# Kernel optimization log

Measured on AMD Instinct MI355X. Metric: run time of the kernel, lower is better.

The kernel has to match this reference:

```python
import jax, jax.numpy as jnp
import numpy as np

N = 30000; E = 480000; B = 32
IN_H = 129; IN_P = 15; HID = 64; HEADS = 8; OUT = 129


def gat_conv(x, src, dst, edge_attr, W, a_src, a_dst, We, a_e, bias, concat):
    # PyG GATConv with edge_dim, add_self_loops=True (fill_value='mean'), negative_slope=0.2
    n = x.shape[0]
    H, C = a_src.shape
    ones = jnp.ones((src.shape[0],), x.dtype)
    deg = jax.ops.segment_sum(ones, dst, num_segments=n)
    ea_mean = jax.ops.segment_sum(edge_attr, dst, num_segments=n) / jnp.clip(deg, 1.0)[:, None]
    loop = jnp.arange(n, dtype=src.dtype)
    s = jnp.concatenate([src, loop])
    t = jnp.concatenate([dst, loop])
    ea = jnp.concatenate([edge_attr, ea_mean], axis=0)
    xw = (x @ W).reshape(n, H, C)              # [N,H,C]
    a_s = jnp.sum(xw * a_src, axis=-1)         # [N,H]
    a_d = jnp.sum(xw * a_dst, axis=-1)         # [N,H]
    ew = (ea @ We).reshape(-1, H, C)           # [E2,H,C]
    a_ed = jnp.sum(ew * a_e, axis=-1)          # [E2,H]
    alpha = jax.nn.leaky_relu(a_s[s] + a_d[t] + a_ed, 0.2)
    amax = jax.ops.segment_max(alpha, t, num_segments=n)   # every node has a self-loop
    expa = jnp.exp(alpha - amax[t])
    denom = jax.ops.segment_sum(expa, t, num_segments=n)
    alpha = expa / denom[t]                    # segment softmax over dst
    out = jax.ops.segment_sum(xw[s] * alpha[..., None], t, num_segments=n)  # [N,H,C]
    out = out.reshape(n, H * C) if concat else jnp.mean(out, axis=1)
    return out + bias


def setup_inputs():
    key = jax.random.key(0)
    ks = jax.random.split(key, 40)
    g = lambda k, s: (jax.random.normal(k, s, jnp.float32) * (1.0 / np.sqrt(s[0])))
    d = {}
    d['x_hrtf'] = jax.random.normal(ks[0], (N, IN_H), jnp.float32)
    d['x_pos'] = jax.random.normal(ks[1], (N, IN_P), jnp.float32)
    d['edge_attr_hrtf'] = jax.random.normal(ks[2], (E, 1), jnp.float32)
    d['edge_attr_pos'] = jax.random.normal(ks[3], (E, 1), jnp.float32)
    # hrtf branch, layer 1 (heads=8, concat)
    d['W1h'] = g(ks[4], (IN_H, HEADS * HID)); d['as1h'] = g(ks[5], (HEADS, HID)); d['ad1h'] = g(ks[6], (HEADS, HID))
    d['We1h'] = g(ks[7], (1, HEADS * HID)); d['ae1h'] = g(ks[8], (HEADS, HID)); d['b1h'] = jnp.zeros((HEADS * HID,), jnp.float32)
    # hrtf branch, layer 2 (heads=1, mean)
    d['W2h'] = g(ks[9], (HEADS * HID, OUT)); d['as2h'] = g(ks[10], (1, OUT)); d['ad2h'] = g(ks[11], (1, OUT))
    d['We2h'] = g(ks[12], (1, OUT)); d['ae2h'] = g(ks[13], (1, OUT)); d['b2h'] = jnp.zeros((OUT,), jnp.float32)
    # pos branch, layer 1
    d['W1p'] = g(ks[14], (IN_P, HEADS * HID)); d['as1p'] = g(ks[15], (HEADS, HID)); d['ad1p'] = g(ks[16], (HEADS, HID))
    d['We1p'] = g(ks[17], (1, HEADS * HID)); d['ae1p'] = g(ks[18], (HEADS, HID)); d['b1p'] = jnp.zeros((HEADS * HID,), jnp.float32)
    # pos branch, layer 2
    d['W2p'] = g(ks[19], (HEADS * HID, OUT)); d['as2p'] = g(ks[20], (1, OUT)); d['ad2p'] = g(ks[21], (1, OUT))
    d['We2p'] = g(ks[22], (1, OUT)); d['ae2p'] = g(ks[23], (1, OUT)); d['b2p'] = jnp.zeros((OUT,), jnp.float32)
    # final fc
    d['Wfc'] = g(ks[24], (2 * OUT, 129)); d['bfc'] = jnp.zeros((129,), jnp.float32)
    d['edge_index_hrtf'] = jax.random.randint(ks[25], (2, E), 0, N, jnp.int32)
    d['edge_index_pos'] = jax.random.randint(ks[26], (2, E), 0, N, jnp.int32)
    d['batch'] = ((jnp.arange(N) * B) // N).astype(jnp.int32)  # sorted, equal-sized graphs
    d['num_graphs'] = B
    return d


def reference(x_hrtf, x_pos, edge_attr_hrtf, edge_attr_pos, W1h, as1h, ad1h, We1h, ae1h, b1h, W2h, as2h, ad2h, We2h, ae2h, b2h, W1p, as1p, ad1p, We1p, ae1p, b1p, W2p, as2p, ad2p, We2p, ae2p, b2p, Wfc, bfc, edge_index_hrtf, edge_index_pos, batch, num_graphs):
    sh, th = edge_index_hrtf[0], edge_index_hrtf[1]
    sp, tp = edge_index_pos[0], edge_index_pos[1]
    h = jax.nn.elu(gat_conv(x_hrtf, sh, th, edge_attr_hrtf, W1h, as1h, ad1h, We1h, ae1h, b1h, True))
    h = gat_conv(h, sh, th, edge_attr_hrtf, W2h, as2h, ad2h, We2h, ae2h, b2h, False)
    p = jax.nn.elu(gat_conv(x_pos, sp, tp, edge_attr_pos, W1p, as1p, ad1p, We1p, ae1p, b1p, True))
    p = gat_conv(p, sp, tp, edge_attr_pos, W2p, as2p, ad2p, We2p, ae2p, b2p, False)
    counts = jax.ops.segment_sum(jnp.ones_like(batch), batch, num_segments=num_graphs)
    last = jnp.cumsum(counts) - 1              # last node index of each graph
    z = jnp.concatenate([h[last], p[last]], axis=-1)
    z = z @ Wfc + bfc
    return z[:, None, :]                       # [B,1,129]
```

## Files before the change

### kernel.cpp

```cpp
#include <hip/hip_runtime.h>

#define N_NODES 30000
#define N_EDGES 480000
#define NB      32
#define HEADS   8
#define F1      512
#define OUT_C   129
#define OUT_S   132
#define W1TS    132

#define CAP1   1024
#define MAXD   64
#define NZREG  (8 + 2 * CAP1 + 2 * NB)
#define TJ     32
#define RB     8

#define SHIFT1 12.0f
#define SHIFT2 20.0f

__device__ __forceinline__ float lrelu(float a) { return a > 0.f ? a : 0.2f * a; }

__device__ __forceinline__ int graph_of(int v) { return (int)(((unsigned)v * 2u) / 1875u); }
__device__ __forceinline__ int last_of(int b) { return (int)((((unsigned)(b + 1) * 1875u) + 1u) / 2u) - 1; }
__device__ __forceinline__ bool is_last_node(int v) { return v == last_of(graph_of(v)); }

__global__ void k_prep(const float* We1h, const float* ae1h,
                       const float* We1p, const float* ae1p,
                       const float* We2h, const float* ae2h,
                       const float* We2p, const float* ae2p,
                       const float* __restrict__ W1h, const float* __restrict__ W1p,
                       const float* __restrict__ W2h, const float* __restrict__ W2p,
                       const float* as1h, const float* as1p,
                       const float* ad1h, const float* ad1p,
                       float* k12, float* __restrict__ w_as, float* __restrict__ w_ad,
                       float* __restrict__ W2t2, int* __restrict__ zreg,
                       int* __restrict__ inv1) {
    int gid = blockIdx.x * 256 + threadIdx.x;
    if (gid < 15000) ((int4*)inv1)[gid] = make_int4(-1, -1, -1, -1);
    if (gid < NZREG) zreg[gid] = 0;
    if (gid < 512 * OUT_C) {
        int k = gid / OUT_C, c = gid % OUT_C;
        W2t2[c * 512 + k] = W2h[gid];
        W2t2[512 * OUT_C + c * 512 + k] = W2p[gid];
    }
    if (blockIdx.x == 0) {
        int t = threadIdx.x;
        if (t < 8) {
            float s = 0.f;
            for (int c = 0; c < 64; c++) s += We1h[t * 64 + c] * ae1h[t * 64 + c];
            k12[t] = s;
        } else if (t < 16) {
            int h = t - 8;
            float s = 0.f;
            for (int c = 0; c < 64; c++) s += We1p[h * 64 + c] * ae1p[h * 64 + c];
            k12[8 + h] = s;
        } else if (t == 16) {
            float s = 0.f;
            for (int c = 0; c < OUT_C; c++) s += We2h[c] * ae2h[c];
            k12[16] = s;
        } else if (t == 17) {
            float s = 0.f;
            for (int c = 0; c < OUT_C; c++) s += We2p[c] * ae2p[c];
            k12[17] = s;
        }
    }
    if (blockIdx.x >= 128 && blockIdx.x < 160) {
        int bb = blockIdx.x - 128;
        int br = bb >> 4, type = (bb >> 3) & 1, h = bb & 7;
        const float* W1 = br ? W1p : W1h;
        const float* a  = type ? (br ? ad1p : ad1h) : (br ? as1p : as1h);
        float* outp = (type ? w_ad : w_as) + (size_t)(br * 8 + h) * W1TS;
        int K = br ? 15 : 129;
        int d = threadIdx.x;
        if (d < K) {
            float s = 0.f;
            for (int c = 0; c < 64; c++) s += W1[(size_t)d * F1 + h * 64 + c] * a[h * 64 + c];
            outp[d] = s;
        }
    }
}

__global__ __launch_bounds__(256) void k_scan2(const int* __restrict__ ei_h,
        const int* __restrict__ ei_p, const float* __restrict__ ea_h,
        const float* __restrict__ ea_p, int* inv1, int* nodes1, int* cnt,
        int* degcnt2, int* eb2v, float* eb2e) {
    __shared__ int s_claim[128];
    __shared__ int s_n, s_base;
    int br = blockIdx.y;
    const int* ei = br ? ei_p : ei_h;
    const float* ea = br ? ea_p : ea_h;
    const int* src = ei; const int* dst = ei + N_EDGES;
    int* inv1b = inv1 + br * N_NODES;
    int* nodes1b = nodes1 + br * CAP1;
    int* cntp = cnt + br * 4;
    int* dc2 = degcnt2 + br * NB;
    int* e2v = eb2v + br * NB * MAXD;
    float* e2e = eb2e + br * NB * MAXD;
    int tid = threadIdx.x;
    if (tid == 0) s_n = 0;
    __syncthreads();
    auto claim = [&](int v) {
        if (atomicCAS(&inv1b[v], -1, -3) == -1) {
            int p = atomicAdd(&s_n, 1);
            if (p < 128) s_claim[p] = v;
            else {
                int j = atomicAdd(cntp, 1);
                if (j < CAP1) { nodes1b[j] = v; inv1b[v] = j; }
                else inv1b[v] = -1;
            }
        }
    };
    if (blockIdx.x == 0 && tid < NB) claim(last_of(tid));
    int base = (blockIdx.x * 256 + tid) * 4;
    if (base < N_EDGES) {
        int4 d4 = *(const int4*)(dst + base);
        int dv[4] = {d4.x, d4.y, d4.z, d4.w};
#pragma unroll
        for (int q = 0; q < 4; q++) {
            if (is_last_node(dv[q])) {
                int e = base + q;
                int b = graph_of(dv[q]);
                int slot = atomicAdd(dc2 + b, 1);
                if (slot < MAXD) { e2v[b * MAXD + slot] = src[e]; e2e[b * MAXD + slot] = ea[e]; }
                claim(src[e]);
            }
        }
    }
    __syncthreads();
    int n = s_n; if (n > 128) n = 128;
    if (tid == 0) s_base = atomicAdd(cntp, n);
    __syncthreads();
    for (int q = tid; q < n; q += 256) {
        int j = s_base + q;
        int v = s_claim[q];
        if (j < CAP1) { nodes1b[j] = v; inv1b[v] = j; }
        else inv1b[v] = -1;
    }
}

__global__ __launch_bounds__(256) void k_scan1(const int* __restrict__ ei_h,
        const int* __restrict__ ei_p, const float* __restrict__ ea_h,
        const float* __restrict__ ea_p, const int* __restrict__ inv1,
        int* degcnt1, int* ebv1, float* ebe1) {
    int br = blockIdx.y;
    const int* ei = br ? ei_p : ei_h;
    const float* ea = br ? ea_p : ea_h;
    const int* src = ei; const int* dst = ei + N_EDGES;
    const int* inv1b = inv1 + br * N_NODES;
    degcnt1 += br * CAP1; ebv1 += (size_t)br * CAP1 * MAXD; ebe1 += (size_t)br * CAP1 * MAXD;
    int tid = threadIdx.x;
    int base = (blockIdx.x * 256 + tid) * 4;
    if (base >= N_EDGES) return;
    int4 d = *(const int4*)(dst + base);
    int dv[4] = {d.x, d.y, d.z, d.w};
#pragma unroll
    for (int q = 0; q < 4; q++) {
        int jj = inv1b[dv[q]];
        if (jj >= 0 && jj < CAP1) {
            int e = base + q;
            int slot = atomicAdd(degcnt1 + jj, 1);
            if (slot < MAXD) { ebv1[jj * MAXD + slot] = src[e]; ebe1[jj * MAXD + slot] = ea[e]; }
        }
    }
}

__global__ __launch_bounds__(256) void k_agg1(const int* __restrict__ ebv1,
        const float* __restrict__ ebe1, const int* __restrict__ degcnt1,
        const int* __restrict__ nodes1, const int* cnt,
        const float* __restrict__ x_h, const float* __restrict__ x_p,
        const float* __restrict__ w_as, const float* __restrict__ w_ad,
        const float* __restrict__ k12, float* __restrict__ xaggn) {
    __shared__ float s_x[MAXD + 1][W1TS];
    __shared__ int   s_v[MAXD + 1];
    __shared__ float s_e[MAXD + 1];
    __shared__ float s_ex[(MAXD + 1) * 8];
    __shared__ float s_den[8];
    __shared__ float s_adh[8];
    __shared__ float s_k1[8];
    int br = blockIdx.y;
    const float* x    = br ? x_p : x_h;
    const float* wasb = w_as + (size_t)br * 8 * W1TS;
    const float* wadb = w_ad + (size_t)br * 8 * W1TS;
    int K = br ? 15 : 129;
    int n1 = cnt[br * 4 + 0]; if (n1 > CAP1) n1 = CAP1;
    int j = blockIdx.x;
    if (j >= n1) return;
    int tid = threadIdx.x;
    int deg = degcnt1[br * CAP1 + j]; if (deg > MAXD) deg = MAXD;
    const int*   ebv = ebv1 + ((size_t)br * CAP1 + j) * MAXD;
    const float* ebe = ebe1 + ((size_t)br * CAP1 + j) * MAXD;
    if (tid < deg) { s_v[tid] = ebv[tid]; s_e[tid] = ebe[tid]; }
    if (tid == 0) s_v[deg] = nodes1[br * CAP1 + j];
    if (tid >= 72 && tid < 80) s_k1[tid - 72] = k12[br * 8 + (tid - 72)];
    __syncthreads();
    int total = deg + 1;
    for (int k = tid >> 6; k < total; k += 4) {
        const float* xr = x + (size_t)s_v[k] * K;
        for (int d = (tid & 63); d < K; d += 64) s_x[k][d] = xr[d];
    }
    __syncthreads();
    if (tid < 64) {
        float part = (tid < deg) ? s_e[tid] : 0.f;
#pragma unroll
        for (int o = 32; o > 0; o >>= 1) part += __shfl_down(part, o);
        if (tid == 0) s_e[deg] = part / fmaxf((float)deg, 1.f);
    }
    for (int t = tid; t < total * 8 + 8; t += 256) {
        int k, h; const float* wv;
        if (t < total * 8) { k = t >> 3; h = t & 7; wv = wasb + (size_t)h * W1TS; }
        else               { k = total - 1; h = t - total * 8; wv = wadb + (size_t)h * W1TS; }
        float dot = 0.f;
        for (int d = 0; d < K; d++) dot += s_x[k][d] * wv[d];
        if (t < total * 8) s_ex[t] = dot; else s_adh[h] = dot;
    }
    __syncthreads();
    for (int t = tid; t < total * 8; t += 256) {
        int k = t >> 3, h = t & 7;
        float a = lrelu(s_ex[t] + s_adh[h] + s_e[k] * s_k1[h]);
        s_ex[t] = __expf(a - SHIFT1);
    }
    __syncthreads();
    if (tid < 8) {
        float d = 0.f;
        for (int k = 0; k < total; k++) d += s_ex[k * 8 + tid];
        s_den[tid] = 1.f / d;
    }
    __syncthreads();
    if (tid < K) {
        float acc[8];
#pragma unroll
        for (int h = 0; h < 8; h++) acc[h] = 0.f;
        for (int k = 0; k < total; k++) {
            float xv = s_x[k][tid];
#pragma unroll
            for (int h = 0; h < 8; h++) acc[h] += s_ex[k * 8 + h] * xv;
        }
#pragma unroll
        for (int h = 0; h < 8; h++)
            xaggn[((size_t)(br * 8 + h) * CAP1 + j) * W1TS + tid] = acc[h] * s_den[h];
    }
}

__global__ __launch_bounds__(256) void k_h1gemm(const float* __restrict__ xaggn,
        const int* cnt, const float* __restrict__ W1h, const float* __restrict__ W1p,
        const float* __restrict__ b1h, const float* __restrict__ b1p,
        float* __restrict__ h1) {
    __shared__ float s_a[TJ][W1TS];
    __shared__ float s_b[OUT_C][64];
    int br = blockIdx.y;
    const float* W1 = br ? W1p : W1h;
    const float* b1 = br ? b1p : b1h;
    int K = br ? 15 : 129;
    int n1 = cnt[br * 4 + 0]; if (n1 > CAP1) n1 = CAP1;
    int jt = blockIdx.x >> 3, h = blockIdx.x & 7;
    int j0 = jt * TJ;
    if (j0 >= n1) return;
    int tid = threadIdx.x;
    const float4* ap = (const float4*)(xaggn + ((size_t)(br * 8 + h) * CAP1 + j0) * W1TS);
    for (int t = tid; t < TJ * W1TS / 4; t += 256) ((float4*)&s_a[0][0])[t] = ap[t];
    for (int t = tid; t < K * 64; t += 256) {
        int d = t >> 6, c = t & 63;
        s_b[d][c] = W1[(size_t)d * F1 + h * 64 + c];
    }
    __syncthreads();
    int r0 = (tid >> 6) * 8, c = tid & 63;
    float acc[8];
#pragma unroll
    for (int rr = 0; rr < 8; rr++) acc[rr] = 0.f;
    for (int d = 0; d < K; d++) {
        float bv = s_b[d][c];
#pragma unroll
        for (int rr = 0; rr < 8; rr++) acc[rr] += s_a[r0 + rr][d] * bv;
    }
    float bb = b1[h * 64 + c];
#pragma unroll
    for (int rr = 0; rr < 8; rr++) {
        int j = j0 + r0 + rr;
        if (j < n1) {
            float v = acc[rr] + bb;
            h1[((size_t)br * CAP1 + j) * F1 + h * 64 + c] = v > 0.f ? v : (__expf(v) - 1.f);
        }
    }
}

__global__ __launch_bounds__(256) void k_gemm2b(const float* __restrict__ h1,
        const float* __restrict__ W2t2, const float* __restrict__ as2h,
        const float* __restrict__ as2p, const float* __restrict__ ad2h,
        const float* __restrict__ ad2p, const int* cnt,
        float* __restrict__ xw2, float* __restrict__ as2v, float* __restrict__ ad2all) {
    __shared__ float hs[RB][512];
    __shared__ float part[4][RB][132];
    __shared__ float rows_[RB][132];
    __shared__ float redS[4][RB], redD[4][RB];
    int br = blockIdx.y;
    const float* W2t = W2t2 + (size_t)br * 512 * OUT_C;
    const float* as2w = br ? as2p : as2h;
    const float* ad2w = br ? ad2p : ad2h;
    h1 += (size_t)br * CAP1 * F1;
    xw2 += (size_t)br * CAP1 * OUT_S;
    as2v += br * CAP1; ad2all += br * CAP1;
    int n1 = cnt[br * 4 + 0]; if (n1 > CAP1) n1 = CAP1;
    int j0 = blockIdx.x * RB;
    if (j0 >= n1) return;
    int tid = threadIdx.x;
    for (int r = 0; r < RB; r++) {
        int j = j0 + r;
        for (int k = tid; k < 512; k += 256)
            hs[r][k] = (j < n1) ? h1[(size_t)j * F1 + k] : 0.f;
    }
    __syncthreads();
    int w = tid >> 6, l = tid & 63;
    float a0[RB], a1[RB], a2[RB];
#pragma unroll
    for (int r = 0; r < RB; r++) { a0[r] = 0.f; a1[r] = 0.f; a2[r] = 0.f; }
    const float* w0p = W2t + (size_t)l * 512;
    const float* w1p = W2t + (size_t)(64 + l) * 512;
    const float* w2p = W2t + (size_t)128 * 512;
    int kbase = w * 128;
#pragma unroll 2
    for (int kk = 0; kk < 128; kk += 4) {
        int k = kbase + kk;
        float4 wv0 = *(const float4*)(w0p + k);
        float4 wv1 = *(const float4*)(w1p + k);
        float4 wv2 = *(const float4*)(w2p + k);
#pragma unroll
        for (int r = 0; r < RB; r++) {
            float4 hv = *(const float4*)&hs[r][k];
            a0[r] += hv.x * wv0.x + hv.y * wv0.y + hv.z * wv0.z + hv.w * wv0.w;
            a1[r] += hv.x * wv1.x + hv.y * wv1.y + hv.z * wv1.z + hv.w * wv1.w;
            a2[r] += hv.x * wv2.x + hv.y * wv2.y + hv.z * wv2.z + hv.w * wv2.w;
        }
    }
#pragma unroll
    for (int r = 0; r < RB; r++) {
        part[w][r][l] = a0[r];
        part[w][r][64 + l] = a1[r];
        if (l == 0) part[w][r][128] = a2[r];
    }
    __syncthreads();
    for (int idx = tid; idx < RB * OUT_C; idx += 256) {
        int r = idx / OUT_C;
        int c = idx - r * OUT_C;
        float s = part[0][r][c] + part[1][r][c] + part[2][r][c] + part[3][r][c];
        rows_[r][c] = s;
        int j = j0 + r;
        if (j < n1) xw2[(size_t)j * OUT_S + c] = s;
    }
    __syncthreads();
#pragma unroll
    for (int t = 0; t < 2; t++) {
        int r = w + t * 4;
        float ps = rows_[r][l] * as2w[l] + rows_[r][64 + l] * as2w[64 + l];
        float pd = rows_[r][l] * ad2w[l] + rows_[r][64 + l] * ad2w[64 + l];
        if (l == 0) { ps += rows_[r][128] * as2w[128]; pd += rows_[r][128] * ad2w[128]; }
#pragma unroll
        for (int o = 32; o > 0; o >>= 1) { ps += __shfl_down(ps, o); pd += __shfl_down(pd, o); }
        if (l == 0) { redS[w][r] = ps; redD[w][r] = pd; }
    }
    __syncthreads();
    if (tid < RB) {
        int j = j0 + tid;
        if (j < n1) {
            int w0 = tid & 3;
            as2v[j] = redS[w0][tid];
            ad2all[j] = redD[w0][tid];
        }
    }
}

__global__ __launch_bounds__(256) void k_agg2fc(const int* __restrict__ eb2v,
        const float* __restrict__ eb2e, const int* __restrict__ degcnt2,
        const int* __restrict__ inv1, const int* cnt,
        const float* __restrict__ as2v, const float* __restrict__ ad2all,
        const float* __restrict__ k12, const float* __restrict__ b2h,
        const float* __restrict__ b2p, const float* __restrict__ xw2,
        const float* __restrict__ Wfc, const float* __restrict__ bfc,
        float* __restrict__ out) {
    __shared__ int   s_j[MAXD + 1];
    __shared__ float s_e[MAXD + 1];
    __shared__ float s_ex[MAXD + 1];
    __shared__ float s_den;
    __shared__ float hcat[2 * OUT_C];
    int b = blockIdx.x;
    int tid = threadIdx.x;
    for (int br = 0; br < 2; br++) {
        const float* b2 = br ? b2p : b2h;
        const int* inv1b = inv1 + br * N_NODES;
        const float* as2vb = as2v + br * CAP1;
        const float* ad2b = ad2all + br * CAP1;
        const float* xw2b = xw2 + (size_t)br * CAP1 * OUT_S;
        float k2 = k12[16 + br];
        int deg = degcnt2[br * NB + b]; if (deg > MAXD) deg = MAXD;
        if (tid < deg) {
            s_j[tid] = inv1b[eb2v[(br * NB + b) * MAXD + tid]];
            s_e[tid] = eb2e[(br * NB + b) * MAXD + tid];
        }
        if (tid == 0) s_j[deg] = inv1b[last_of(b)];
        __syncthreads();
        if (tid < 64) {
            float part = (tid < deg) ? s_e[tid] : 0.f;
#pragma unroll
            for (int o = 32; o > 0; o >>= 1) part += __shfl_down(part, o);
            if (tid == 0) s_e[deg] = part / fmaxf((float)deg, 1.f);
        }
        __syncthreads();
        int total = deg + 1;
        float adv = ad2b[s_j[deg]];
        for (int k = tid; k < total; k += 256)
            s_ex[k] = __expf(lrelu(as2vb[s_j[k]] + adv + s_e[k] * k2) - SHIFT2);
        __syncthreads();
        if (tid == 0) {
            float d = 0.f;
            for (int k = 0; k < total; k++) d += s_ex[k];
            s_den = d;
        }
        __syncthreads();
        if (tid < OUT_C) {
            float acc = 0.f;
            for (int k = 0; k < total; k++)
                acc += s_ex[k] * xw2b[(size_t)s_j[k] * OUT_S + tid];
            hcat[br * OUT_C + tid] = acc / s_den + b2[tid];
        }
        __syncthreads();
    }
    if (tid < OUT_C) {
        float s = bfc[tid];
        for (int k = 0; k < 2 * OUT_C; k++) s += hcat[k] * Wfc[k * OUT_C + tid];
        out[b * OUT_C + tid] = s;
    }
}

extern "C" void kernel_launch(void* const* d_in, const int* in_sizes, int n_in,
                              void* d_out, int out_size, void* d_ws, size_t ws_size,
                              hipStream_t stream) {
    const float* x_h  = (const float*)d_in[0];
    const float* x_p  = (const float*)d_in[1];
    const float* ea_h = (const float*)d_in[2];
    const float* ea_p = (const float*)d_in[3];
    const float* W1h  = (const float*)d_in[4];
    const float* as1h = (const float*)d_in[5];
    const float* ad1h = (const float*)d_in[6];
    const float* We1h = (const float*)d_in[7];
    const float* ae1h = (const float*)d_in[8];
    const float* b1h  = (const float*)d_in[9];
    const float* W2h  = (const float*)d_in[10];
    const float* as2h = (const float*)d_in[11];
    const float* ad2h = (const float*)d_in[12];
    const float* We2h = (const float*)d_in[13];
    const float* ae2h = (const float*)d_in[14];
    const float* b2h  = (const float*)d_in[15];
    const float* W1p  = (const float*)d_in[16];
    const float* as1p = (const float*)d_in[17];
    const float* ad1p = (const float*)d_in[18];
    const float* We1p = (const float*)d_in[19];
    const float* ae1p = (const float*)d_in[20];
    const float* b1p  = (const float*)d_in[21];
    const float* W2p  = (const float*)d_in[22];
    const float* as2p = (const float*)d_in[23];
    const float* ad2p = (const float*)d_in[24];
    const float* We2p = (const float*)d_in[25];
    const float* ae2p = (const float*)d_in[26];
    const float* b2p  = (const float*)d_in[27];
    const float* Wfc  = (const float*)d_in[28];
    const float* bfc  = (const float*)d_in[29];
    const int*   ei_h = (const int*)d_in[30];
    const int*   ei_p = (const int*)d_in[31];

    char* wsb = (char*)d_ws;
    size_t off = 0;
    auto alloc = [&](size_t elems) -> char* {
        char* p = wsb + off;
        off += ((elems * 4 + 255) / 256) * 256;
        return p;
    };
    float*    k12     = (float*)alloc(18);
    int*      zreg    = (int*)alloc(NZREG);
    int*      cnt     = zreg;
    int*      degcnt1 = zreg + 8;
    int*      degcnt2 = zreg + 8 + 2 * CAP1;
    int*      inv1    = (int*)alloc(2 * N_NODES);
    int*      nodes1  = (int*)alloc(2 * CAP1);
    int*      ebv1    = (int*)alloc(2 * (size_t)CAP1 * MAXD);
    float*    ebe1    = (float*)alloc(2 * (size_t)CAP1 * MAXD);
    int*      eb2v    = (int*)alloc(2 * NB * MAXD);
    float*    eb2e    = (float*)alloc(2 * NB * MAXD);
    float*    w_as    = (float*)alloc(2 * 8 * W1TS);
    float*    w_ad    = (float*)alloc(2 * 8 * W1TS);
    float*    xaggn   = (float*)alloc(2 * 8 * (size_t)CAP1 * W1TS);
    float*    h1      = (float*)alloc(2 * (size_t)CAP1 * F1);
    float*    W2t2    = (float*)alloc(2 * 512 * OUT_C);
    float*    xw2     = (float*)alloc(2 * (size_t)CAP1 * OUT_S);
    float*    as2v    = (float*)alloc(2 * CAP1);
    float*    ad2all  = (float*)alloc(2 * CAP1);
    if (off > ws_size) return;

    const int EBLK4 = (N_EDGES / 4 + 255) / 256;

    k_prep<<<259, 256, 0, stream>>>(
        We1h, ae1h, We1p, ae1p, We2h, ae2h, We2p, ae2p,
        W1h, W1p, W2h, W2p, as1h, as1p, ad1h, ad1p,
        k12, w_as, w_ad, W2t2, zreg, inv1);
    k_scan2<<<dim3(EBLK4, 2), 256, 0, stream>>>(ei_h, ei_p, ea_h, ea_p, inv1,
                                                nodes1, cnt, degcnt2, eb2v, eb2e);
    k_scan1<<<dim3(EBLK4, 2), 256, 0, stream>>>(ei_h, ei_p, ea_h, ea_p, inv1,
                                                degcnt1, ebv1, ebe1);
    k_agg1<<<dim3(CAP1, 2), 256, 0, stream>>>(ebv1, ebe1, degcnt1, nodes1, cnt,
                                              x_h, x_p, w_as, w_ad, k12, xaggn);
    k_h1gemm<<<dim3((CAP1 / TJ) * 8, 2), 256, 0, stream>>>(xaggn, cnt, W1h, W1p,
                                                           b1h, b1p, h1);
    k_gemm2b<<<dim3(CAP1 / RB, 2), 256, 0, stream>>>(h1, W2t2, as2h, as2p, ad2h, ad2p,
                                                     cnt, xw2, as2v, ad2all);
    k_agg2fc<<<NB, 256, 0, stream>>>(eb2v, eb2e, degcnt2, inv1, cnt,
                                     as2v, ad2all, k12, b2h, b2p, xw2, Wfc, bfc, (float*)d_out);
}
```

Baseline: 109.7 us.

## Fuse layer-1 GEMM with layer-2 GEMM and fold prep work into scan kernel

Merges the h1 GEMM and the second-layer GEMM into one kernel that keeps each 8-row tile of h1 in shared memory, so the h1 global buffer and the W2 transpose are no longer needed. The W1 attention-vector and edge-constant precomputation moves into extra blocks of the scan1 kernel, and the init kernel shrinks to just zeroing. This removes one launch and a global round trip of h1. In exchange, each block recomputes W1 tiles per head with less reuse across rows, and reads W2 untransposed from global with scalar loads.

```diff
diff --git a/kernel.cpp b/kernel.cpp
--- a/kernel.cpp
+++ b/kernel.cpp
@@ -12,75 +12,26 @@
 #define CAP1   1024
 #define MAXD   64
 #define NZREG  (8 + 2 * CAP1 + 2 * NB)
-#define TJ     32
-#define RB     8
+#define TJ2    8
+#define H1S    514
 
 #define SHIFT1 12.0f
 #define SHIFT2 20.0f
 
 __device__ __forceinline__ float lrelu(float a) { return a > 0.f ? a : 0.2f * a; }
+__device__ __forceinline__ float elu1(float v) { return v > 0.f ? v : (__expf(v) - 1.f); }
 
 __device__ __forceinline__ int graph_of(int v) { return (int)(((unsigned)v * 2u) / 1875u); }
 __device__ __forceinline__ int last_of(int b) { return (int)((((unsigned)(b + 1) * 1875u) + 1u) / 2u) - 1; }
 __device__ __forceinline__ bool is_last_node(int v) { return v == last_of(graph_of(v)); }
 
-__global__ void k_prep(const float* We1h, const float* ae1h,
-                       const float* We1p, const float* ae1p,
-                       const float* We2h, const float* ae2h,
-                       const float* We2p, const float* ae2p,
-                       const float* __restrict__ W1h, const float* __restrict__ W1p,
-                       const float* __restrict__ W2h, const float* __restrict__ W2p,
-                       const float* as1h, const float* as1p,
-                       const float* ad1h, const float* ad1p,
-                       float* k12, float* __restrict__ w_as, float* __restrict__ w_ad,
-                       float* __restrict__ W2t2, int* __restrict__ zreg,
-                       int* __restrict__ inv1) {
+__global__ void k_init(int* __restrict__ zreg, int* __restrict__ inv1) {
     int gid = blockIdx.x * 256 + threadIdx.x;
     if (gid < 15000) ((int4*)inv1)[gid] = make_int4(-1, -1, -1, -1);
     if (gid < NZREG) zreg[gid] = 0;
-    if (gid < 512 * OUT_C) {
-        int k = gid / OUT_C, c = gid % OUT_C;
-        W2t2[c * 512 + k] = W2h[gid];
-        W2t2[512 * OUT_C + c * 512 + k] = W2p[gid];
-    }
-    if (blockIdx.x == 0) {
-        int t = threadIdx.x;
-        if (t < 8) {
-            float s = 0.f;
-            for (int c = 0; c < 64; c++) s += We1h[t * 64 + c] * ae1h[t * 64 + c];
-            k12[t] = s;
-        } else if (t < 16) {
-            int h = t - 8;
-            float s = 0.f;
-            for (int c = 0; c < 64; c++) s += We1p[h * 64 + c] * ae1p[h * 64 + c];
-            k12[8 + h] = s;
-        } else if (t == 16) {
-            float s = 0.f;
-            for (int c = 0; c < OUT_C; c++) s += We2h[c] * ae2h[c];
-            k12[16] = s;
-        } else if (t == 17) {
-            float s = 0.f;
-            for (int c = 0; c < OUT_C; c++) s += We2p[c] * ae2p[c];
-            k12[17] = s;
-        }
-    }
-    if (blockIdx.x >= 128 && blockIdx.x < 160) {
-        int bb = blockIdx.x - 128;
-        int br = bb >> 4, type = (bb >> 3) & 1, h = bb & 7;
-        const float* W1 = br ? W1p : W1h;
-        const float* a  = type ? (br ? ad1p : ad1h) : (br ? as1p : as1h);
-        float* outp = (type ? w_ad : w_as) + (size_t)(br * 8 + h) * W1TS;
-        int K = br ? 15 : 129;
-        int d = threadIdx.x;
-        if (d < K) {
-            float s = 0.f;
-            for (int c = 0; c < 64; c++) s += W1[(size_t)d * F1 + h * 64 + c] * a[h * 64 + c];
-            outp[d] = s;
-        }
-    }
-}
-
-__global__ __launch_bounds__(256) void k_scan2(const int* __restrict__ ei_h,
+}
+
+__global__ __launch_bounds__(256) void k_scan2c(const int* __restrict__ ei_h,
         const int* __restrict__ ei_p, const float* __restrict__ ea_h,
         const float* __restrict__ ea_p, int* inv1, int* nodes1, int* cnt,
         int* degcnt2, int* eb2v, float* eb2e) {
@@ -138,18 +89,62 @@
     }
 }
 
-__global__ __launch_bounds__(256) void k_scan1(const int* __restrict__ ei_h,
+__global__ __launch_bounds__(256) void k_scan1w(const int* __restrict__ ei_h,
         const int* __restrict__ ei_p, const float* __restrict__ ea_h,
         const float* __restrict__ ea_p, const int* __restrict__ inv1,
-        int* degcnt1, int* ebv1, float* ebe1) {
+        int* degcnt1, int* ebv1, float* ebe1,
+        const float* __restrict__ W1h, const float* __restrict__ W1p,
+        const float* as1h, const float* as1p,
+        const float* ad1h, const float* ad1p,
+        const float* We1h, const float* ae1h, const float* We1p, const float* ae1p,
+        const float* We2h, const float* ae2h, const float* We2p, const float* ae2p,
+        float* __restrict__ w_as, float* __restrict__ w_ad, float* __restrict__ k12) {
+    const int EBLK4 = (N_EDGES / 4 + 255) / 256;
     int br = blockIdx.y;
+    int chunk = blockIdx.x;
+    int tid = threadIdx.x;
+    if (chunk >= EBLK4) {
+        int ex = chunk - EBLK4;
+        if (ex < 16) {
+            int type = ex >> 3, h = ex & 7;
+            const float* W1 = br ? W1p : W1h;
+            const float* a  = type ? (br ? ad1p : ad1h) : (br ? as1p : as1h);
+            float* outp = (type ? w_ad : w_as) + (size_t)(br * 8 + h) * W1TS;
+            int K = br ? 15 : 129;
+            if (tid < K) {
+                float s = 0.f;
+                for (int c = 0; c < 64; c++) s += W1[(size_t)tid * F1 + h * 64 + c] * a[h * 64 + c];
+                outp[tid] = s;
+            }
+        } else if (br == 0) {
+            int t = tid;
+            if (t < 8) {
+                float s = 0.f;
+                for (int c = 0; c < 64; c++) s += We1h[t * 64 + c] * ae1h[t * 64 + c];
+                k12[t] = s;
+            } else if (t < 16) {
+                int h = t - 8;
+                float s = 0.f;
+                for (int c = 0; c < 64; c++) s += We1p[h * 64 + c] * ae1p[h * 64 + c];
+                k12[8 + h] = s;
+            } else if (t == 16) {
+                float s = 0.f;
+                for (int c = 0; c < OUT_C; c++) s += We2h[c] * ae2h[c];
+                k12[16] = s;
+            } else if (t == 17) {
+                float s = 0.f;
+                for (int c = 0; c < OUT_C; c++) s += We2p[c] * ae2p[c];
+                k12[17] = s;
+            }
+        }
+        return;
+    }
     const int* ei = br ? ei_p : ei_h;
     const float* ea = br ? ea_p : ea_h;
     const int* src = ei; const int* dst = ei + N_EDGES;
     const int* inv1b = inv1 + br * N_NODES;
     degcnt1 += br * CAP1; ebv1 += (size_t)br * CAP1 * MAXD; ebe1 += (size_t)br * CAP1 * MAXD;
-    int tid = threadIdx.x;
-    int base = (blockIdx.x * 256 + tid) * 4;
+    int base = (chunk * 256 + tid) * 4;
     if (base >= N_EDGES) return;
     int4 d = *(const int4*)(dst + base);
     int dv[4] = {d.x, d.y, d.z, d.w};
@@ -241,129 +236,114 @@
     }
 }
 
-__global__ __launch_bounds__(256) void k_h1gemm(const float* __restrict__ xaggn,
-        const int* cnt, const float* __restrict__ W1h, const float* __restrict__ W1p,
+__global__ __launch_bounds__(256) void k_h1x2(const float* __restrict__ xaggn,
+        const int* cnt,
+        const float* __restrict__ W1h, const float* __restrict__ W1p,
         const float* __restrict__ b1h, const float* __restrict__ b1p,
-        float* __restrict__ h1) {
-    __shared__ float s_a[TJ][W1TS];
-    __shared__ float s_b[OUT_C][64];
+        const float* __restrict__ W2h, const float* __restrict__ W2p,
+        const float* __restrict__ as2h, const float* __restrict__ as2p,
+        const float* __restrict__ ad2h, const float* __restrict__ ad2p,
+        float* __restrict__ xw2, float* __restrict__ as2v, float* __restrict__ ad2all) {
+    __shared__ float s_h1[TJ2 * H1S];
+    __shared__ float ubuf[5280];
+    __shared__ float redS[4][TJ2], redD[4][TJ2];
     int br = blockIdx.y;
-    const float* W1 = br ? W1p : W1h;
-    const float* b1 = br ? b1p : b1h;
+    const float* W1   = br ? W1p : W1h;
+    const float* b1   = br ? b1p : b1h;
+    const float* W2   = br ? W2p : W2h;
+    const float* as2w = br ? as2p : as2h;
+    const float* ad2w = br ? ad2p : ad2h;
     int K = br ? 15 : 129;
-    int n1 = cnt[br * 4 + 0]; if (n1 > CAP1) n1 = CAP1;
-    int jt = blockIdx.x >> 3, h = blockIdx.x & 7;
-    int j0 = jt * TJ;
+    int n1 = cnt[br * 4]; if (n1 > CAP1) n1 = CAP1;
+    int j0 = blockIdx.x * TJ2;
     if (j0 >= n1) return;
     int tid = threadIdx.x;
-    const float4* ap = (const float4*)(xaggn + ((size_t)(br * 8 + h) * CAP1 + j0) * W1TS);
-    for (int t = tid; t < TJ * W1TS / 4; t += 256) ((float4*)&s_a[0][0])[t] = ap[t];
-    for (int t = tid; t < K * 64; t += 256) {
-        int d = t >> 6, c = t & 63;
-        s_b[d][c] = W1[(size_t)d * F1 + h * 64 + c];
-    }
-    __syncthreads();
-    int r0 = (tid >> 6) * 8, c = tid & 63;
-    float acc[8];
-#pragma unroll
-    for (int rr = 0; rr < 8; rr++) acc[rr] = 0.f;
-    for (int d = 0; d < K; d++) {
-        float bv = s_b[d][c];
-#pragma unroll
-        for (int rr = 0; rr < 8; rr++) acc[rr] += s_a[r0 + rr][d] * bv;
-    }
-    float bb = b1[h * 64 + c];
-#pragma unroll
-    for (int rr = 0; rr < 8; rr++) {
-        int j = j0 + r0 + rr;
-        if (j < n1) {
-            float v = acc[rr] + bb;
-            h1[((size_t)br * CAP1 + j) * F1 + h * 64 + c] = v > 0.f ? v : (__expf(v) - 1.f);
-        }
-    }
-}
-
-__global__ __launch_bounds__(256) void k_gemm2b(const float* __restrict__ h1,
-        const float* __restrict__ W2t2, const float* __restrict__ as2h,
-        const float* __restrict__ as2p, const float* __restrict__ ad2h,
-        const float* __restrict__ ad2p, const int* cnt,
-        float* __restrict__ xw2, float* __restrict__ as2v, float* __restrict__ ad2all) {
-    __shared__ float hs[RB][512];
-    __shared__ float part[4][RB][132];
-    __shared__ float rows_[RB][132];
-    __shared__ float redS[4][RB], redD[4][RB];
-    int br = blockIdx.y;
-    const float* W2t = W2t2 + (size_t)br * 512 * OUT_C;
-    const float* as2w = br ? as2p : as2h;
-    const float* ad2w = br ? ad2p : ad2h;
-    h1 += (size_t)br * CAP1 * F1;
-    xw2 += (size_t)br * CAP1 * OUT_S;
-    as2v += br * CAP1; ad2all += br * CAP1;
-    int n1 = cnt[br * 4 + 0]; if (n1 > CAP1) n1 = CAP1;
-    int j0 = blockIdx.x * RB;
-    if (j0 >= n1) return;
-    int tid = threadIdx.x;
-    for (int r = 0; r < RB; r++) {
+    int w = tid >> 6, l = tid & 63;
+
+    float* s_a = ubuf;
+    float* s_b = ubuf + 1056;
+    int r0 = (tid >> 6) * 2, c = tid & 63;
+    for (int h = 0; h < 8; h++) {
+        __syncthreads();
+        const float4* ap = (const float4*)(xaggn + ((size_t)(br * 8 + h) * CAP1 + j0) * W1TS);
+        for (int t = tid; t < TJ2 * W1TS / 4; t += 256) ((float4*)s_a)[t] = ap[t];
+        float acc0 = 0.f, acc1 = 0.f;
+        for (int d0 = 0; d0 < K; d0 += 65) {
+            int dn = K - d0; if (dn > 65) dn = 65;
+            __syncthreads();
+            for (int t = tid; t < dn * 64; t += 256) {
+                int d = t >> 6, cc = t & 63;
+                s_b[d * 64 + cc] = W1[(size_t)(d0 + d) * F1 + h * 64 + cc];
+            }
+            __syncthreads();
+            for (int d = 0; d < dn; d++) {
+                float bv = s_b[d * 64 + c];
+                acc0 += s_a[r0 * W1TS + d0 + d] * bv;
+                acc1 += s_a[(r0 + 1) * W1TS + d0 + d] * bv;
+            }
+        }
+        float bb = b1[h * 64 + c];
+        s_h1[r0 * H1S + h * 64 + c]       = elu1(acc0 + bb);
+        s_h1[(r0 + 1) * H1S + h * 64 + c] = elu1(acc1 + bb);
+    }
+    __syncthreads();
+
+    float* s_part = ubuf;
+    {
+        float a0[TJ2], a1[TJ2], a2[TJ2];
+#pragma unroll
+        for (int r = 0; r < TJ2; r++) { a0[r] = 0.f; a1[r] = 0.f; a2[r] = 0.f; }
+        int k0 = w * 128;
+        for (int kk = 0; kk < 128; kk++) {
+            int k = k0 + kk;
+            float w2a = W2[(size_t)k * OUT_C + l];
+            float w2b = W2[(size_t)k * OUT_C + 64 + l];
+            float w2c = (l == 0) ? W2[(size_t)k * OUT_C + 128] : 0.f;
+#pragma unroll
+            for (int r = 0; r < TJ2; r++) {
+                float hv = s_h1[r * H1S + k];
+                a0[r] += hv * w2a;
+                a1[r] += hv * w2b;
+                a2[r] += hv * w2c;
+            }
+        }
+#pragma unroll
+        for (int r = 0; r < TJ2; r++) {
+            s_part[(w * TJ2 + r) * 132 + l] = a0[r];
+            s_part[(w * TJ2 + r) * 132 + 64 + l] = a1[r];
+            if (l == 0) s_part[(w * TJ2 + r) * 132 + 128] = a2[r];
+        }
+    }
+    __syncthreads();
+    float* rows_ = ubuf + 4224;
+    for (int idx = tid; idx < TJ2 * OUT_C; idx += 256) {
+        int r = idx / OUT_C;
+        int cc = idx - r * OUT_C;
+        float s = s_part[(0 * TJ2 + r) * 132 + cc] + s_part[(1 * TJ2 + r) * 132 + cc]
+                + s_part[(2 * TJ2 + r) * 132 + cc] + s_part[(3 * TJ2 + r) * 132 + cc];
+        rows_[r * 132 + cc] = s;
         int j = j0 + r;
-        for (int k = tid; k < 512; k += 256)
-            hs[r][k] = (j < n1) ? h1[(size_t)j * F1 + k] : 0.f;
-    }
-    __syncthreads();
-    int w = tid >> 6, l = tid & 63;
-    float a0[RB], a1[RB], a2[RB];
-#pragma unroll
-    for (int r = 0; r < RB; r++) { a0[r] = 0.f; a1[r] = 0.f; a2[r] = 0.f; }
-    const float* w0p = W2t + (size_t)l * 512;
-    const float* w1p = W2t + (size_t)(64 + l) * 512;
-    const float* w2p = W2t + (size_t)128 * 512;
-    int kbase = w * 128;
-#pragma unroll 2
-    for (int kk = 0; kk < 128; kk += 4) {
-        int k = kbase + kk;
-        float4 wv0 = *(const float4*)(w0p + k);
-        float4 wv1 = *(const float4*)(w1p + k);
-        float4 wv2 = *(const float4*)(w2p + k);
-#pragma unroll
-        for (int r = 0; r < RB; r++) {
-            float4 hv = *(const float4*)&hs[r][k];
-            a0[r] += hv.x * wv0.x + hv.y * wv0.y + hv.z * wv0.z + hv.w * wv0.w;
-            a1[r] += hv.x * wv1.x + hv.y * wv1.y + hv.z * wv1.z + hv.w * wv1.w;
-            a2[r] += hv.x * wv2.x + hv.y * wv2.y + hv.z * wv2.z + hv.w * wv2.w;
-        }
-    }
-#pragma unroll
-    for (int r = 0; r < RB; r++) {
-        part[w][r][l] = a0[r];
-        part[w][r][64 + l] = a1[r];
-        if (l == 0) part[w][r][128] = a2[r];
-    }
-    __syncthreads();
-    for (int idx = tid; idx < RB * OUT_C; idx += 256) {
-        int r = idx / OUT_C;
-        int c = idx - r * OUT_C;
-        float s = part[0][r][c] + part[1][r][c] + part[2][r][c] + part[3][r][c];
-        rows_[r][c] = s;
-        int j = j0 + r;
-        if (j < n1) xw2[(size_t)j * OUT_S + c] = s;
-    }
-    __syncthreads();
+        if (j < n1) xw2[((size_t)br * CAP1 + j) * OUT_S + cc] = s;
+    }
+    __syncthreads();
+
 #pragma unroll
     for (int t = 0; t < 2; t++) {
         int r = w + t * 4;
-        float ps = rows_[r][l] * as2w[l] + rows_[r][64 + l] * as2w[64 + l];
-        float pd = rows_[r][l] * ad2w[l] + rows_[r][64 + l] * ad2w[64 + l];
-        if (l == 0) { ps += rows_[r][128] * as2w[128]; pd += rows_[r][128] * ad2w[128]; }
+        float ps = rows_[r * 132 + l] * as2w[l] + rows_[r * 132 + 64 + l] * as2w[64 + l];
+        float pd = rows_[r * 132 + l] * ad2w[l] + rows_[r * 132 + 64 + l] * ad2w[64 + l];
+        if (l == 0) { ps += rows_[r * 132 + 128] * as2w[128]; pd += rows_[r * 132 + 128] * ad2w[128]; }
 #pragma unroll
         for (int o = 32; o > 0; o >>= 1) { ps += __shfl_down(ps, o); pd += __shfl_down(pd, o); }
         if (l == 0) { redS[w][r] = ps; redD[w][r] = pd; }
     }
     __syncthreads();
-    if (tid < RB) {
+    if (tid < TJ2) {
         int j = j0 + tid;
         if (j < n1) {
             int w0 = tid & 3;
-            as2v[j] = redS[w0][tid];
-            ad2all[j] = redD[w0][tid];
+            as2v[br * CAP1 + j] = redS[w0][tid];
+            ad2all[br * CAP1 + j] = redD[w0][tid];
         }
     }
 }
@@ -487,8 +467,6 @@
     float*    w_as    = (float*)alloc(2 * 8 * W1TS);
     float*    w_ad    = (float*)alloc(2 * 8 * W1TS);
     float*    xaggn   = (float*)alloc(2 * 8 * (size_t)CAP1 * W1TS);
-    float*    h1      = (float*)alloc(2 * (size_t)CAP1 * F1);
-    float*    W2t2    = (float*)alloc(2 * 512 * OUT_C);
     float*    xw2     = (float*)alloc(2 * (size_t)CAP1 * OUT_S);
     float*    as2v    = (float*)alloc(2 * CAP1);
     float*    ad2all  = (float*)alloc(2 * CAP1);
@@ -496,20 +474,20 @@
 
     const int EBLK4 = (N_EDGES / 4 + 255) / 256;
 
-    k_prep<<<259, 256, 0, stream>>>(
-        We1h, ae1h, We1p, ae1p, We2h, ae2h, We2p, ae2p,
-        W1h, W1p, W2h, W2p, as1h, as1p, ad1h, ad1p,
-        k12, w_as, w_ad, W2t2, zreg, inv1);
-    k_scan2<<<dim3(EBLK4, 2), 256, 0, stream>>>(ei_h, ei_p, ea_h, ea_p, inv1,
-                                                nodes1, cnt, degcnt2, eb2v, eb2e);
-    k_scan1<<<dim3(EBLK4, 2), 256, 0, stream>>>(ei_h, ei_p, ea_h, ea_p, inv1,
-                                                degcnt1, ebv1, ebe1);
+    k_init<<<59, 256, 0, stream>>>(zreg, inv1);
+    k_scan2c<<<dim3(EBLK4, 2), 256, 0, stream>>>(ei_h, ei_p, ea_h, ea_p, inv1,
+                                                 nodes1, cnt, degcnt2, eb2v, eb2e);
+    k_scan1w<<<dim3(EBLK4 + 17, 2), 256, 0, stream>>>(ei_h, ei_p, ea_h, ea_p, inv1,
+                                                      degcnt1, ebv1, ebe1,
+                                                      W1h, W1p, as1h, as1p, ad1h, ad1p,
+                                                      We1h, ae1h, We1p, ae1p,
+                                                      We2h, ae2h, We2p, ae2p,
+                                                      w_as, w_ad, k12);
     k_agg1<<<dim3(CAP1, 2), 256, 0, stream>>>(ebv1, ebe1, degcnt1, nodes1, cnt,
                                               x_h, x_p, w_as, w_ad, k12, xaggn);
-    k_h1gemm<<<dim3((CAP1 / TJ) * 8, 2), 256, 0, stream>>>(xaggn, cnt, W1h, W1p,
-                                                           b1h, b1p, h1);
-    k_gemm2b<<<dim3(CAP1 / RB, 2), 256, 0, stream>>>(h1, W2t2, as2h, as2p, ad2h, ad2p,
-                                                     cnt, xw2, as2v, ad2all);
+    k_h1x2<<<dim3(CAP1 / TJ2, 2), 256, 0, stream>>>(xaggn, cnt, W1h, W1p, b1h, b1p,
+                                                    W2h, W2p, as2h, as2p, ad2h, ad2p,
+                                                    xw2, as2v, ad2all);
     k_agg2fc<<<NB, 256, 0, stream>>>(eb2v, eb2e, degcnt2, inv1, cnt,
                                      as2v, ad2all, k12, b2h, b2p, xw2, Wfc, bfc, (float*)d_out);
 }
```

Result: slower. 137.8 us (+25.5%).
